# Kernel tuning notes

Hardware: AMD Instinct MI355X
Metric: run time of the kernel (lower is better)

## Reference

```python
import jax, jax.numpy as jnp
import numpy as np

S, B, T = 512, 512, 64


def setup_inputs() -> dict:
    key = jax.random.key(0)
    k1, k2, k3, k4, k5 = jax.random.split(key, 5)
    emissions = jax.random.normal(k1, (S, B, T), dtype=jnp.float32)
    tags = jax.random.randint(k2, (S, B), 0, T, dtype=jnp.int64)
    mask = jnp.ones((S, B), dtype=jnp.bool_)
    # parameters: uniform(-0.1, 0.1) as in _reset_parameters
    start_transitions = jax.random.uniform(k3, (T,), minval=-0.1, maxval=0.1, dtype=jnp.float32)
    end_transitions = jax.random.uniform(k4, (T,), minval=-0.1, maxval=0.1, dtype=jnp.float32)
    transitions = jax.random.uniform(k5, (T, T), minval=-0.1, maxval=0.1, dtype=jnp.float32)
    return {
        "emissions": emissions,
        "tags": tags,
        "mask": mask,
        "start_transitions": start_transitions,
        "end_transitions": end_transitions,
        "transitions": transitions,
    }


def _crf_llh(emissions, tags, mask, start_transitions, end_transitions, transitions):
    # emissions: [S, B, T]; tags: [S, B] int; mask: [S, B] bool (time-major)
    s, b_sz, _ = emissions.shape
    b = jnp.arange(b_sz)
    maskf = mask.astype(emissions.dtype)

    # ----- numerator: score of the given tag path -----
    score = start_transitions[tags[0]] + emissions[0, b, tags[0]]  # [B]
    trans_step = transitions[tags[:-1], tags[1:]]                  # [S-1, B]
    em_step = jnp.take_along_axis(emissions, tags[..., None], axis=2)[..., 0]  # [S, B]
    score = score + jnp.sum((trans_step + em_step[1:]) * maskf[1:], axis=0)
    seq_ends = mask.astype(jnp.int32).sum(axis=0) - 1              # [B]
    last_tags = tags[seq_ends, b]
    numerator = score + end_transitions[last_tags]                 # [B]

    # ----- denominator: forward-algorithm log partition -----
    def step(alpha, xs):
        em_i, m_i = xs  # [B, T], [B]
        # alpha[b, i] + transitions[i, j] + em_i[b, j] -> logsumexp over i
        nxt = jax.nn.logsumexp(alpha[:, :, None] + transitions[None, :, :] + em_i[:, None, :], axis=1)
        return jnp.where(m_i[:, None], nxt, alpha), None

    alpha0 = start_transitions + emissions[0]  # [B, T]
    alpha, _ = jax.lax.scan(step, alpha0, (emissions[1:], mask[1:]))
    denominator = jax.nn.logsumexp(alpha + end_transitions, axis=1)  # [B]

    llh = numerator - denominator
    return llh.mean()  # reduction='mean' (the default)


def reference(emissions, tags, mask, start_transitions, end_transitions, transitions):
    return _crf_llh(emissions, tags, mask, start_transitions, end_transitions, transitions)
```

## Files before the change

kernel.cpp:

```cpp
#include <hip/hip_runtime.h>
#include <math.h>

#define SS 512
#define BB 512
#define TT 64
#define GRP 8

__device__ __forceinline__ float bl0(float x) {
    return __int_as_float(__builtin_amdgcn_readfirstlane(__float_as_int(x)));
}

__global__ __launch_bounds__(64) void crf_chains(
    const float* __restrict__ em,
    const int*   __restrict__ tags,
    const int*   __restrict__ mask,
    const float* __restrict__ start_t,
    const float* __restrict__ end_t,
    const float* __restrict__ trans,
    float* __restrict__ alpha_mid,
    float* __restrict__ beta_mid,
    float* __restrict__ num_ws)
{
    const int lane = threadIdx.x;
    const int bid  = blockIdx.x;
    __shared__ float lds[TT * 65];

    if (bid < BB) {
        const int b = bid;
        const float* embase = em + (size_t)b * TT + lane;
        const int*   mkbase = mask + b;

        float e[TT];
        #pragma unroll
        for (int i = 0; i < TT; ++i)
            e[i] = __expf(trans[i * TT + lane]);

        float alpha = start_t[lane] + embase[0];

        float em0[GRP], em1[GRP];
        int   mk0[GRP], mk1[GRP];

        auto LOADF = [&](float* eb, int* mb, int g) {
            const int sb = 1 + g * GRP;
            #pragma unroll
            for (int k = 0; k < GRP; ++k) {
                eb[k] = embase[(size_t)(sb + k) * BB * TT];
                mb[k] = mkbase[(sb + k) * BB];
            }
        };
        auto STEPSF = [&](const float* eb, const int* mb, bool lastg) {
            #pragma unroll
            for (int k = 0; k < GRP; ++k) {
                const int par = (k & 1) * TT;
                float off = bl0(alpha);
                float p   = __expf(alpha - off);
                lds[par + lane] = p;
                float a0 = 0.f, a1 = 0.f, a2 = 0.f, a3 = 0.f;
                #pragma unroll
                for (int i = 0; i < 16; ++i) {
                    float4 pv = *(const float4*)&lds[par + i * 4];
                    a0 += pv.x * e[4 * i + 0];
                    a1 += pv.y * e[4 * i + 1];
                    a2 += pv.z * e[4 * i + 2];
                    a3 += pv.w * e[4 * i + 3];
                }
                float acc = (a0 + a1) + (a2 + a3);
                float na  = eb[k] + off + __logf(acc);
                int mk = mb[k];
                if (k == GRP - 1) mk = lastg ? 0 : mk;
                alpha = mk ? na : alpha;
            }
        };

        LOADF(em0, mk0, 0);
        LOADF(em1, mk1, 1);
        for (int gg = 0; gg < 32; gg += 2) {
            STEPSF(em0, mk0, false);
            LOADF(em0, mk0, gg + 2);
            STEPSF(em1, mk1, gg + 1 == 31);
            LOADF(em1, mk1, gg + 3);
        }
        alpha_mid[(size_t)b * TT + lane] = alpha;

    } else if (bid < 2 * BB) {
        const int b = bid - BB;
        const float* embase = em + (size_t)b * TT + lane;
        const int*   mkbase = mask + b;

        for (int k = 0; k < TT; ++k)
            lds[k * 65 + lane] = trans[k * TT + lane];
        float e[TT];
        #pragma unroll
        for (int j = 0; j < TT; ++j)
            e[j] = __expf(lds[lane * 65 + j]);

        float beta = end_t[lane];

        float em0[GRP], em1[GRP];
        int   mk0[GRP], mk1[GRP];

        auto LOADB = [&](float* eb, int* mb, int g) {
            const int sb = 511 - g * GRP;
            #pragma unroll
            for (int k = 0; k < GRP; ++k) {
                eb[k] = embase[(size_t)(sb - k) * BB * TT];
                mb[k] = mkbase[(sb - k) * BB];
            }
        };
        auto STEPSB = [&](const float* eb, const int* mb) {
            #pragma unroll
            for (int k = 0; k < GRP; ++k) {
                const int par = (k & 1) * TT;
                float qa  = eb[k] + beta;
                float off = bl0(qa);
                float q   = __expf(qa - off);
                lds[par + lane] = q;
                float a0 = 0.f, a1 = 0.f, a2 = 0.f, a3 = 0.f;
                #pragma unroll
                for (int j = 0; j < 16; ++j) {
                    float4 qv = *(const float4*)&lds[par + j * 4];
                    a0 += qv.x * e[4 * j + 0];
                    a1 += qv.y * e[4 * j + 1];
                    a2 += qv.z * e[4 * j + 2];
                    a3 += qv.w * e[4 * j + 3];
                }
                float acc = (a0 + a1) + (a2 + a3);
                float nb  = off + __logf(acc);
                beta = mb[k] ? nb : beta;
            }
        };

        LOADB(em0, mk0, 0);
        LOADB(em1, mk1, 1);
        for (int gg = 0; gg < 32; gg += 2) {
            STEPSB(em0, mk0);
            LOADB(em0, mk0, gg + 2);
            STEPSB(em1, mk1);
            LOADB(em1, mk1, gg + 3);
        }
        beta_mid[(size_t)b * TT + lane] = beta;

    } else {
        const int b = bid - 2 * BB;
        float local = 0.f;
        int   mcnt  = 0;
        for (int s = lane; s < SS; s += 64) {
            int tag = tags[s * BB + b];
            int mk  = mask[s * BB + b];
            mcnt += mk;
            if (s == 0) {
                local += start_t[tag] + em[(size_t)b * TT + tag];
            } else if (mk) {
                int tp = tags[(s - 1) * BB + b];
                local += trans[tp * TT + tag] + em[(size_t)s * BB * TT + (size_t)b * TT + tag];
            }
        }
        #pragma unroll
        for (int d = 32; d > 0; d >>= 1) {
            local += __shfl_down(local, d, 64);
            mcnt  += __shfl_down(mcnt, d, 64);
        }
        if (lane == 0) {
            int last = tags[(mcnt - 1) * BB + b];
            num_ws[b] = local + end_t[last];
        }
    }
}

__global__ __launch_bounds__(64) void crf_llh(
    const float* __restrict__ alpha_mid,
    const float* __restrict__ beta_mid,
    const float* __restrict__ num_ws,
    float* __restrict__ llh)
{
    const int b = blockIdx.x, lane = threadIdx.x;
    float v = alpha_mid[(size_t)b * TT + lane] + beta_mid[(size_t)b * TT + lane];
    float mx = v;
    #pragma unroll
    for (int d = 32; d > 0; d >>= 1) mx = fmaxf(mx, __shfl_xor(mx, d, 64));
    float s = __expf(v - mx);
    #pragma unroll
    for (int d = 32; d > 0; d >>= 1) s += __shfl_xor(s, d, 64);
    if (lane == 0) llh[b] = num_ws[b] - (mx + __logf(s));
}

__global__ __launch_bounds__(512) void crf_mean(const float* __restrict__ llh,
                                               float* __restrict__ out)
{
    const int t = threadIdx.x;
    float v = llh[t];
    #pragma unroll
    for (int d = 32; d > 0; d >>= 1) v += __shfl_down(v, d, 64);
    __shared__ float red[8];
    if ((t & 63) == 0) red[t >> 6] = v;
    __syncthreads();
    if (t == 0) {
        float s = 0.f;
        #pragma unroll
        for (int w = 0; w < 8; ++w) s += red[w];
        out[0] = s / (float)BB;
    }
}

extern "C" void kernel_launch(void* const* d_in, const int* in_sizes, int n_in,
                              void* d_out, int out_size, void* d_ws, size_t ws_size,
                              hipStream_t stream) {
    const float* em    = (const float*)d_in[0];
    const int*   tags  = (const int*)d_in[1];
    const int*   mask  = (const int*)d_in[2];
    const float* st    = (const float*)d_in[3];
    const float* en    = (const float*)d_in[4];
    const float* tr    = (const float*)d_in[5];

    float* ws        = (float*)d_ws;
    float* alpha_mid = ws;
    float* beta_mid  = ws + (size_t)BB * TT;
    float* num_ws    = ws + (size_t)2 * BB * TT;
    float* llh       = ws + (size_t)2 * BB * TT + BB;

    crf_chains<<<3 * BB, 64, 0, stream>>>(em, tags, mask, st, en, tr,
                                          alpha_mid, beta_mid, num_ws);
    crf_llh<<<BB, 64, 0, stream>>>(alpha_mid, beta_mid, num_ws, llh);
    crf_mean<<<1, 512, 0, stream>>>(llh, (float*)d_out);
}
```

Baseline: 191.0 us.

## Broadcast chain probabilities via readlane and fuse finishing kernels into one

```diff
diff --git a/kernel.cpp b/kernel.cpp
--- a/kernel.cpp
+++ b/kernel.cpp
@@ -8,6 +8,21 @@
 
 __device__ __forceinline__ float bl0(float x) {
     return __int_as_float(__builtin_amdgcn_readfirstlane(__float_as_int(x)));
+}
+__device__ __forceinline__ float rlane(float x, int i) {
+    return __int_as_float(__builtin_amdgcn_readlane(__float_as_int(x), i));
+}
+
+__device__ __forceinline__ float matvec64(float p, const float* e) {
+    float a0 = 0.f, a1 = 0.f, a2 = 0.f, a3 = 0.f;
+    #pragma unroll
+    for (int i = 0; i < 16; ++i) {
+        a0 = fmaf(rlane(p, i     ), e[i     ], a0);
+        a1 = fmaf(rlane(p, i + 16), e[i + 16], a1);
+        a2 = fmaf(rlane(p, i + 32), e[i + 32], a2);
+        a3 = fmaf(rlane(p, i + 48), e[i + 48], a3);
+    }
+    return (a0 + a1) + (a2 + a3);
 }
 
 __global__ __launch_bounds__(64) void crf_chains(
@@ -51,20 +66,9 @@
         auto STEPSF = [&](const float* eb, const int* mb, bool lastg) {
             #pragma unroll
             for (int k = 0; k < GRP; ++k) {
-                const int par = (k & 1) * TT;
                 float off = bl0(alpha);
                 float p   = __expf(alpha - off);
-                lds[par + lane] = p;
-                float a0 = 0.f, a1 = 0.f, a2 = 0.f, a3 = 0.f;
-                #pragma unroll
-                for (int i = 0; i < 16; ++i) {
-                    float4 pv = *(const float4*)&lds[par + i * 4];
-                    a0 += pv.x * e[4 * i + 0];
-                    a1 += pv.y * e[4 * i + 1];
-                    a2 += pv.z * e[4 * i + 2];
-                    a3 += pv.w * e[4 * i + 3];
-                }
-                float acc = (a0 + a1) + (a2 + a3);
+                float acc = matvec64(p, e);
                 float na  = eb[k] + off + __logf(acc);
                 int mk = mb[k];
                 if (k == GRP - 1) mk = lastg ? 0 : mk;
@@ -110,21 +114,10 @@
         auto STEPSB = [&](const float* eb, const int* mb) {
             #pragma unroll
             for (int k = 0; k < GRP; ++k) {
-                const int par = (k & 1) * TT;
                 float qa  = eb[k] + beta;
                 float off = bl0(qa);
                 float q   = __expf(qa - off);
-                lds[par + lane] = q;
-                float a0 = 0.f, a1 = 0.f, a2 = 0.f, a3 = 0.f;
-                #pragma unroll
-                for (int j = 0; j < 16; ++j) {
-                    float4 qv = *(const float4*)&lds[par + j * 4];
-                    a0 += qv.x * e[4 * j + 0];
-                    a1 += qv.y * e[4 * j + 1];
-                    a2 += qv.z * e[4 * j + 2];
-                    a3 += qv.w * e[4 * j + 3];
-                }
-                float acc = (a0 + a1) + (a2 + a3);
+                float acc = matvec64(q, e);
                 float nb  = off + __logf(acc);
                 beta = mb[k] ? nb : beta;
             }
@@ -167,38 +160,33 @@
     }
 }
 
-__global__ __launch_bounds__(64) void crf_llh(
+__global__ __launch_bounds__(512) void crf_finish(
     const float* __restrict__ alpha_mid,
     const float* __restrict__ beta_mid,
     const float* __restrict__ num_ws,
-    float* __restrict__ llh)
+    float* __restrict__ out)
 {
-    const int b = blockIdx.x, lane = threadIdx.x;
-    float v = alpha_mid[(size_t)b * TT + lane] + beta_mid[(size_t)b * TT + lane];
-    float mx = v;
-    #pragma unroll
-    for (int d = 32; d > 0; d >>= 1) mx = fmaxf(mx, __shfl_xor(mx, d, 64));
-    float s = __expf(v - mx);
-    #pragma unroll
-    for (int d = 32; d > 0; d >>= 1) s += __shfl_xor(s, d, 64);
-    if (lane == 0) llh[b] = num_ws[b] - (mx + __logf(s));
-}
-
-__global__ __launch_bounds__(512) void crf_mean(const float* __restrict__ llh,
-                                               float* __restrict__ out)
-{
-    const int t = threadIdx.x;
-    float v = llh[t];
-    #pragma unroll
-    for (int d = 32; d > 0; d >>= 1) v += __shfl_down(v, d, 64);
+    const int lane = threadIdx.x & 63;
+    const int w    = threadIdx.x >> 6;
+    float acc = 0.f;
+    for (int b = w * 64; b < (w + 1) * 64; ++b) {
+        float v = alpha_mid[(size_t)b * TT + lane] + beta_mid[(size_t)b * TT + lane];
+        float mx = v;
+        #pragma unroll
+        for (int d = 32; d > 0; d >>= 1) mx = fmaxf(mx, __shfl_xor(mx, d, 64));
+        float s = __expf(v - mx);
+        #pragma unroll
+        for (int d = 32; d > 0; d >>= 1) s += __shfl_xor(s, d, 64);
+        if (lane == 0) acc += num_ws[b] - (mx + __logf(s));
+    }
     __shared__ float red[8];
-    if ((t & 63) == 0) red[t >> 6] = v;
+    if (lane == 0) red[w] = acc;
     __syncthreads();
-    if (t == 0) {
-        float s = 0.f;
-        #pragma unroll
-        for (int w = 0; w < 8; ++w) s += red[w];
-        out[0] = s / (float)BB;
+    if (threadIdx.x == 0) {
+        float t = 0.f;
+        #pragma unroll
+        for (int i = 0; i < 8; ++i) t += red[i];
+        out[0] = t / (float)BB;
     }
 }
 
@@ -216,10 +204,8 @@
     float* alpha_mid = ws;
     float* beta_mid  = ws + (size_t)BB * TT;
     float* num_ws    = ws + (size_t)2 * BB * TT;
-    float* llh       = ws + (size_t)2 * BB * TT + BB;
 
     crf_chains<<<3 * BB, 64, 0, stream>>>(em, tags, mask, st, en, tr,
                                           alpha_mid, beta_mid, num_ws);
-    crf_llh<<<BB, 64, 0, stream>>>(alpha_mid, beta_mid, num_ws, llh);
-    crf_mean<<<1, 512, 0, stream>>>(llh, (float*)d_out);
-}
+    crf_finish<<<1, 512, 0, stream>>>(alpha_mid, beta_mid, num_ws, (float*)d_out);
+}
```

Result: slower. 207.3 us (+8.6%).
